# Kernel optimization log

Measured on AMD Instinct MI355X. Metric: run time of the kernel, lower is better.

## Reference

```python
import jax, jax.numpy as jnp
import numpy as np

N_NODES = 50000
N_EDGES = 600000
IN_CH = 300
HID = 128
N_CLASSES = 2
N_GRAPHS = 128
BN_EPS = 1e-5


def setup_inputs() -> dict:
    key = jax.random.key(0)
    ks = jax.random.split(key, 24)
    x = jax.random.normal(ks[0], (N_NODES, IN_CH), dtype=jnp.float32)
    edge_index = jax.random.randint(ks[1], (2, N_EDGES), 0, N_NODES, dtype=jnp.int64)
    batch = jnp.sort(jax.random.randint(ks[2], (N_NODES,), 0, N_GRAPHS, dtype=jnp.int64))

    def glorot(k, shape):
        fan_in, fan_out = shape
        s = jnp.sqrt(2.0 / (fan_in + fan_out)).astype(jnp.float32)
        return jax.random.normal(k, shape, dtype=jnp.float32) * s

    inp = {"x": x, "edge_index": edge_index, "batch": batch}
    # SAGEConv params: W_l (neighbor branch), W_r (root branch), bias
    dims = [(IN_CH, HID), (HID, HID), (HID, HID)]
    for i, (din, dout) in enumerate(dims, start=1):
        inp[f"W{i}l"] = glorot(ks[3 * i], (din, dout))
        inp[f"W{i}r"] = glorot(ks[3 * i + 1], (din, dout))
        inp[f"b{i}"] = jnp.zeros((dout,), dtype=jnp.float32)
        inp[f"g{i}"] = jnp.ones((dout,), dtype=jnp.float32)   # BN gamma
        inp[f"be{i}"] = jnp.zeros((dout,), dtype=jnp.float32)  # BN beta
    inp["Wc"] = glorot(ks[20], (HID, N_CLASSES))
    inp["bc"] = jnp.zeros((N_CLASSES,), dtype=jnp.float32)
    return inp


def _sage_conv(x, src, dst, Wl, Wr, b):
    # mean-aggregate neighbor features (messages flow src -> dst)
    msg_sum = jax.ops.segment_sum(x[src], dst, num_segments=N_NODES)
    deg = jax.ops.segment_sum(jnp.ones((src.shape[0],), dtype=x.dtype), dst,
                              num_segments=N_NODES)
    mean = msg_sum / jnp.maximum(deg, 1.0)[:, None]
    return mean @ Wl + x @ Wr + b


def _bn_relu(h, gamma, beta):
    mu = jnp.mean(h, axis=0)
    var = jnp.var(h, axis=0)
    h = (h - mu) * jax.lax.rsqrt(var + BN_EPS) * gamma + beta
    return jax.nn.relu(h)


def reference(x, edge_index, batch,
              W1l, W1r, b1, g1, be1,
              W2l, W2r, b2, g2, be2,
              W3l, W3r, b3, g3, be3,
              Wc, bc):
    src, dst = edge_index[0], edge_index[1]
    h = _bn_relu(_sage_conv(x, src, dst, W1l, W1r, b1), g1, be1)
    h = _bn_relu(_sage_conv(h, src, dst, W2l, W2r, b2), g2, be2)
    h = _bn_relu(_sage_conv(h, src, dst, W3l, W3r, b3), g3, be3)
    # global mean pool per graph
    pooled = jax.ops.segment_sum(h, batch, num_segments=N_GRAPHS)
    cnt = jax.ops.segment_sum(jnp.ones((h.shape[0],), dtype=h.dtype), batch,
                              num_segments=N_GRAPHS)
    hg = pooled / jnp.maximum(cnt, 1.0)[:, None]
    out = hg @ Wc + bc
    return out, hg
```

## Files before the change

kernel.cpp:

```cpp
#include <hip/hip_runtime.h>

#define N_NODES   50000
#define N_EDGES   600000
#define IN_CH     300
#define HID       128
#define N_CLASSES 2
#define N_GRAPHS  128
#define BN_EPS    1e-5f

#define NB ((N_NODES + 511) / 512)
#define KP1 320
#define NREP 32
#define DEGB ((N_EDGES + 255) / 256)
#define GEMMX_BLOCKS ((N_NODES + 63) / 64)
#define FILLB ((N_EDGES + 255) / 256)

typedef __attribute__((ext_vector_type(8))) short bf8_t;
typedef __attribute__((ext_vector_type(4))) float f4_t;

__device__ __forceinline__ unsigned short f2bf(float x) {
    union { float f; unsigned u; } q; q.f = x;
    unsigned r = q.u + 0x7fffu + ((q.u >> 16) & 1u);
    return (unsigned short)(r >> 16);
}
__device__ __forceinline__ float bf2f(unsigned short h) {
    union { float f; unsigned u; } q; q.u = ((unsigned)h) << 16; return q.f;
}

__global__ __launch_bounds__(256) void deg_prepw(const int* __restrict__ dst,
                                                 int* __restrict__ ideg,
                                                 const float* __restrict__ W1l,
                                                 const float* __restrict__ W1r,
                                                 const float* __restrict__ W2l,
                                                 const float* __restrict__ W2r,
                                                 const float* __restrict__ W3l,
                                                 const float* __restrict__ W3r,
                                                 unsigned short* __restrict__ B1h,
                                                 unsigned short* __restrict__ B1l,
                                                 unsigned short* __restrict__ B2h,
                                                 unsigned short* __restrict__ B2l,
                                                 unsigned short* __restrict__ B3h,
                                                 unsigned short* __restrict__ B3l) {
    int b = blockIdx.x;
    if (b < DEGB) {
        int e = b * 256 + threadIdx.x;
        if (e < N_EDGES) atomicAdd(&ideg[dst[e]], 1);
        return;
    }
    int pb = b - DEGB;
    int layer, base;
    if (pb < 320)      { layer = 0; base = pb; }
    else if (pb < 448) { layer = 1; base = pb - 320; }
    else               { layer = 2; base = pb - 448; }
    int Kp = (layer == 0) ? KP1 : HID;
    int K  = (layer == 0) ? IN_CH : HID;
    const float* Wl = (layer == 0) ? W1l : ((layer == 1) ? W2l : W3l);
    const float* Wr = (layer == 0) ? W1r : ((layer == 1) ? W2r : W3r);
    unsigned short* Bh = (layer == 0) ? B1h : ((layer == 1) ? B2h : B3h);
    unsigned short* Bl = (layer == 0) ? B1l : ((layer == 1) ? B2l : B3l);
    int idx = base * 256 + threadIdx.x;
    int n = idx / Kp;
    int k = idx - n * Kp;
    float v = 0.f;
    if (k < K) v = (n < 128) ? Wl[k * 128 + n] : Wr[k * 128 + (n - 128)];
    unsigned short h = f2bf(v);
    unsigned short l = f2bf(v - bf2f(h));
    int NST   = Kp >> 5;
    int ntile = n >> 4;
    int l16n  = n & 15;
    int kstep = k >> 5;
    int kk    = k & 31;
    int lane2 = (kk >> 3) * 16 + l16n;
    int addr  = ((ntile * NST + kstep) * 64 + lane2) * 8 + (kk & 7);
    Bh[addr] = h;
    Bl[addr] = l;
}

__global__ __launch_bounds__(256) void scan_fused(const int* __restrict__ ideg,
                                                  int* __restrict__ row_start,
                                                  float* __restrict__ invdeg,
                                                  int* __restrict__ bsum,
                                                  int* __restrict__ bflag) {
    int b = blockIdx.x, t = threadIdx.x;
    int lane = t & 63, wv = t >> 6;
    int i0 = b * 512 + t * 2;
    int v0 = 0, v1 = 0;
    if (i0 < N_NODES) {
        int2 v = *(const int2*)&ideg[i0];
        v0 = v.x; v1 = v.y;
    }
    int tot = v0 + v1;
    int s = tot;
#pragma unroll
    for (int d = 1; d < 64; d <<= 1) {
        int u = __shfl_up(s, d);
        if (lane >= d) s += u;
    }
    __shared__ int ws[4];
    if (lane == 63) ws[wv] = s;
    __syncthreads();
    int btot = ws[0] + ws[1] + ws[2] + ws[3];
    if (t == 0) {
        atomicExch(&bsum[b], btot);
        __threadfence();
        atomicExch(&bflag[b], 1);
    }
    int part = 0;
    if (t < b) {
        while (atomicAdd(&bflag[t], 0) == 0) {}
        part = atomicAdd(&bsum[t], 0);
    }
#pragma unroll
    for (int d = 1; d < 64; d <<= 1) part += __shfl_down(part, d);
    __shared__ int ps[4];
    if (lane == 0) ps[wv] = part;
    __syncthreads();
    int boff = ps[0] + ps[1] + ps[2] + ps[3];
    int woff = 0;
    for (int w = 0; w < wv; ++w) woff += ws[w];
    int base = boff + woff + (s - tot);
    if (i0 < N_NODES) {
        row_start[i0]     = base;
        row_start[i0 + 1] = base + v0;
        invdeg[i0]     = 1.0f / fmaxf((float)v0, 1.0f);
        invdeg[i0 + 1] = 1.0f / fmaxf((float)v1, 1.0f);
    }
    if (t == 0 && b == NB - 1) row_start[N_NODES] = boff + btot;
}

__global__ __launch_bounds__(256) void gemm_x_fill(const float* __restrict__ X,
                                                   int M,
                                                   const unsigned short* __restrict__ Bhi,
                                                   const unsigned short* __restrict__ Blo,
                                                   const float* __restrict__ bias,
                                                   unsigned short* __restrict__ C0,
                                                   float* __restrict__ C1,
                                                   const int* __restrict__ esrc,
                                                   const int* __restrict__ edst,
                                                   const int* __restrict__ row_start,
                                                   int* __restrict__ cursor,
                                                   int* __restrict__ csr_src) {
    if (blockIdx.x >= GEMMX_BLOCKS) {
        int e = (blockIdx.x - GEMMX_BLOCKS) * 256 + threadIdx.x;
        if (e < N_EDGES) {
            int d = edst[e];
            int pos = row_start[d] + atomicAdd(&cursor[d], 1);
            csr_src[pos] = esrc[e];
        }
        return;
    }

    __shared__ __align__(16) unsigned short sAh[2][64 * 32];
    __shared__ __align__(16) unsigned short sAl[2][64 * 32];

    const int tid  = threadIdx.x;
    const int lane = tid & 63;
    const int wave = tid >> 6;
    const int l16  = lane & 15;
    const int quad = lane >> 4;
    const long m0  = (long)blockIdx.x * 64;
    const int  n0  = wave * 64;

    f4_t acc[4][4];
#pragma unroll
    for (int mt = 0; mt < 4; ++mt)
#pragma unroll
        for (int nt = 0; nt < 4; ++nt) acc[mt][nt] = (f4_t){0.f, 0.f, 0.f, 0.f};

    const int ar  = tid >> 2;
    const int cl  = tid & 3;
    const int cpa = cl ^ ((ar >> 1) & 3);
    long agr = m0 + ar;
    if (agr >= M) agr = M - 1;
    const float* gX = X + agr * IN_CH;

    const int rsw = (quad ^ ((l16 >> 1) & 3)) * 8;
    const int NT  = KP1 / 32;

    const bf8_t* Bh0 = (const bf8_t*)Bhi;
    const bf8_t* Bl0 = (const bf8_t*)Blo;

    auto loadA = [&](int k0, float4& a0, float4& a1) {
        int gk = k0 + cl * 8;
        a0 = (gk + 4 <= IN_CH) ? *(const float4*)(gX + gk)
                               : make_float4(0.f, 0.f, 0.f, 0.f);
        a1 = (gk + 8 <= IN_CH) ? *(const float4*)(gX + gk + 4)
                               : make_float4(0.f, 0.f, 0.f, 0.f);
    };
    auto storeA = [&](int buf, float4 a0, float4 a1) {
        float f[8];
        f[0] = a0.x; f[1] = a0.y; f[2] = a0.z; f[3] = a0.w;
        f[4] = a1.x; f[5] = a1.y; f[6] = a1.z; f[7] = a1.w;
        bf8_t h8, l8;
#pragma unroll
        for (int j = 0; j < 8; ++j) {
            unsigned short h = f2bf(f[j]);
            h8[j] = (short)h;
            l8[j] = (short)f2bf(f[j] - bf2f(h));
        }
        *(bf8_t*)&sAh[buf][ar * 32 + cpa * 8] = h8;
        *(bf8_t*)&sAl[buf][ar * 32 + cpa * 8] = l8;
    };
    auto loadB = [&](int t, bf8_t (&bh)[4], bf8_t (&bl)[4]) {
#pragma unroll
        for (int nt = 0; nt < 4; ++nt) {
            long bi = ((long)(wave * 4 + nt) * NT + t) * 64 + lane;
            bh[nt] = Bh0[bi];
            bl[nt] = Bl0[bi];
        }
    };

    bf8_t bhv[4], blv[4];
    {
        float4 a0, a1;
        loadA(0, a0, a1);
        loadB(0, bhv, blv);
        storeA(0, a0, a1);
    }
    __syncthreads();

    int cur = 0;
    for (int t = 0; t < NT; ++t) {
        float4 na0 = make_float4(0.f, 0.f, 0.f, 0.f);
        float4 na1 = make_float4(0.f, 0.f, 0.f, 0.f);
        bf8_t nbh[4], nbl[4];
        const bool more = (t + 1 < NT);
        if (more) {
            loadA((t + 1) * 32, na0, na1);
            loadB(t + 1, nbh, nbl);
        }

        bf8_t ah[4], al[4];
#pragma unroll
        for (int mt = 0; mt < 4; ++mt) {
            ah[mt] = *(const bf8_t*)&sAh[cur][(mt * 16 + l16) * 32 + rsw];
            al[mt] = *(const bf8_t*)&sAl[cur][(mt * 16 + l16) * 32 + rsw];
        }
#pragma unroll
        for (int nt = 0; nt < 4; ++nt)
#pragma unroll
            for (int mt = 0; mt < 4; ++mt)
                acc[mt][nt] = __builtin_amdgcn_mfma_f32_16x16x32_bf16(ah[mt], bhv[nt], acc[mt][nt], 0, 0, 0);
#pragma unroll
        for (int nt = 0; nt < 4; ++nt)
#pragma unroll
            for (int mt = 0; mt < 4; ++mt)
                acc[mt][nt] = __builtin_amdgcn_mfma_f32_16x16x32_bf16(al[mt], bhv[nt], acc[mt][nt], 0, 0, 0);
#pragma unroll
        for (int nt = 0; nt < 4; ++nt)
#pragma unroll
            for (int mt = 0; mt < 4; ++mt)
                acc[mt][nt] = __builtin_amdgcn_mfma_f32_16x16x32_bf16(ah[mt], blv[nt], acc[mt][nt], 0, 0, 0);

        if (more) {
            storeA(cur ^ 1, na0, na1);
#pragma unroll
            for (int nt = 0; nt < 4; ++nt) {
                bhv[nt] = nbh[nt];
                blv[nt] = nbl[nt];
            }
        }
        __syncthreads();
        cur ^= 1;
    }

    const bool left = (n0 < 128);
    if (left) {
        int ncol[4];
#pragma unroll
        for (int nt = 0; nt < 4; ++nt) ncol[nt] = n0 + nt * 16 + l16;
#pragma unroll
        for (int mt = 0; mt < 4; ++mt)
#pragma unroll
            for (int r = 0; r < 4; ++r) {
                long row = m0 + mt * 16 + quad * 4 + r;
                if (row < M) {
#pragma unroll
                    for (int nt = 0; nt < 4; ++nt)
                        C0[row * 128 + ncol[nt]] = f2bf(acc[mt][nt][r]);
                }
            }
    } else {
        float badd[4];
        int   ncol[4];
#pragma unroll
        for (int nt = 0; nt < 4; ++nt) {
            int ng = n0 + nt * 16 + l16 - 128;
            ncol[nt] = ng;
            badd[nt] = bias[ng];
        }
#pragma unroll
        for (int mt = 0; mt < 4; ++mt)
#pragma unroll
            for (int r = 0; r < 4; ++r) {
                long row = m0 + mt * 16 + quad * 4 + r;
                if (row < M) {
#pragma unroll
                    for (int nt = 0; nt < 4; ++nt)
                        C1[row * 128 + ncol[nt]] = acc[mt][nt][r] + badd[nt];
                }
            }
    }
}

__global__ __launch_bounds__(256) void gemm_mfma_h(const float* __restrict__ Hpre,
                                                   int M,
                                                   const float* __restrict__ rep,
                                                   const float* __restrict__ gamma,
                                                   const float* __restrict__ beta,
                                                   const unsigned short* __restrict__ Bhi,
                                                   const unsigned short* __restrict__ Blo,
                                                   const float* __restrict__ bias,
                                                   unsigned short* __restrict__ C0,
                                                   float* __restrict__ C1) {
    __shared__ __align__(16) unsigned short sAh[2][64 * 32];
    __shared__ __align__(16) unsigned short sAl[2][64 * 32];
    __shared__ float sSC[256];

    const int tid  = threadIdx.x;
    const int lane = tid & 63;
    const int wave = tid >> 6;
    const int l16  = lane & 15;
    const int quad = lane >> 4;
    const long m0  = (long)blockIdx.x * 64;
    const int  n0  = wave * 64;

    {
        float* S = (float*)sAh;
        float a = 0.f;
#pragma unroll
        for (int r = 0; r < NREP; ++r) a += rep[r * 256 + tid];
        S[tid] = a;
        __syncthreads();
        if (tid < HID) {
            const float invn = 1.0f / (float)N_NODES;
            float mu  = S[tid] * invn;
            float var = S[HID + tid] * invn - mu * mu;
            float sc  = gamma[tid] * rsqrtf(var + BN_EPS);
            sSC[tid]       = sc;
            sSC[HID + tid] = beta[tid] - mu * sc;
        }
        __syncthreads();
    }

    f4_t acc[4][4];
#pragma unroll
    for (int mt = 0; mt < 4; ++mt)
#pragma unroll
        for (int nt = 0; nt < 4; ++nt) acc[mt][nt] = (f4_t){0.f, 0.f, 0.f, 0.f};

    const int ar  = tid >> 2;
    const int cl  = tid & 3;
    const int cpa = cl ^ ((ar >> 1) & 3);
    long agr = m0 + ar;
    if (agr >= M) agr = M - 1;
    const float* gH = Hpre + agr * HID;

    const int rsw = (quad ^ ((l16 >> 1) & 3)) * 8;
    const int NT  = HID / 32;

    const bf8_t* Bh0 = (const bf8_t*)Bhi;
    const bf8_t* Bl0 = (const bf8_t*)Blo;

    auto loadA = [&](int k0, float4& a0, float4& a1) {
        int gk = k0 + cl * 8;
        a0 = *(const float4*)(gH + gk);
        a1 = *(const float4*)(gH + gk + 4);
    };
    auto storeA = [&](int buf, int k0, float4 v0, float4 v1) {
        const int gk = k0 + cl * 8;
        float4 s0 = *(const float4*)&sSC[gk];
        float4 s1 = *(const float4*)&sSC[gk + 4];
        float4 t0 = *(const float4*)&sSC[HID + gk];
        float4 t1 = *(const float4*)&sSC[HID + gk + 4];
        float f[8];
        f[0] = fmaxf(v0.x * s0.x + t0.x, 0.f);
        f[1] = fmaxf(v0.y * s0.y + t0.y, 0.f);
        f[2] = fmaxf(v0.z * s0.z + t0.z, 0.f);
        f[3] = fmaxf(v0.w * s0.w + t0.w, 0.f);
        f[4] = fmaxf(v1.x * s1.x + t1.x, 0.f);
        f[5] = fmaxf(v1.y * s1.y + t1.y, 0.f);
        f[6] = fmaxf(v1.z * s1.z + t1.z, 0.f);
        f[7] = fmaxf(v1.w * s1.w + t1.w, 0.f);
        bf8_t h8, l8;
#pragma unroll
        for (int j = 0; j < 8; ++j) {
            unsigned short h = f2bf(f[j]);
            h8[j] = (short)h;
            l8[j] = (short)f2bf(f[j] - bf2f(h));
        }
        *(bf8_t*)&sAh[buf][ar * 32 + cpa * 8] = h8;
        *(bf8_t*)&sAl[buf][ar * 32 + cpa * 8] = l8;
    };
    auto loadB = [&](int t, bf8_t (&bh)[4], bf8_t (&bl)[4]) {
#pragma unroll
        for (int nt = 0; nt < 4; ++nt) {
            long bi = ((long)(wave * 4 + nt) * NT + t) * 64 + lane;
            bh[nt] = Bh0[bi];
            bl[nt] = Bl0[bi];
        }
    };

    bf8_t bhv[4], blv[4];
    {
        float4 a0, a1;
        loadA(0, a0, a1);
        loadB(0, bhv, blv);
        storeA(0, 0, a0, a1);
    }
    __syncthreads();

    int cur = 0;
#pragma unroll
    for (int t = 0; t < 4; ++t) {
        float4 na0 = make_float4(0.f, 0.f, 0.f, 0.f);
        float4 na1 = make_float4(0.f, 0.f, 0.f, 0.f);
        bf8_t nbh[4], nbl[4];
        const bool more = (t < 3);
        if (more) {
            loadA((t + 1) * 32, na0, na1);
            loadB(t + 1, nbh, nbl);
        }

        bf8_t ah[4], al[4];
#pragma unroll
        for (int mt = 0; mt < 4; ++mt) {
            ah[mt] = *(const bf8_t*)&sAh[cur][(mt * 16 + l16) * 32 + rsw];
            al[mt] = *(const bf8_t*)&sAl[cur][(mt * 16 + l16) * 32 + rsw];
        }
#pragma unroll
        for (int nt = 0; nt < 4; ++nt)
#pragma unroll
            for (int mt = 0; mt < 4; ++mt)
                acc[mt][nt] = __builtin_amdgcn_mfma_f32_16x16x32_bf16(ah[mt], bhv[nt], acc[mt][nt], 0, 0, 0);
#pragma unroll
        for (int nt = 0; nt < 4; ++nt)
#pragma unroll
            for (int mt = 0; mt < 4; ++mt)
                acc[mt][nt] = __builtin_amdgcn_mfma_f32_16x16x32_bf16(al[mt], bhv[nt], acc[mt][nt], 0, 0, 0);
#pragma unroll
        for (int nt = 0; nt < 4; ++nt)
#pragma unroll
            for (int mt = 0; mt < 4; ++mt)
                acc[mt][nt] = __builtin_amdgcn_mfma_f32_16x16x32_bf16(ah[mt], blv[nt], acc[mt][nt], 0, 0, 0);

        if (more) {
            storeA(cur ^ 1, (t + 1) * 32, na0, na1);
#pragma unroll
            for (int nt = 0; nt < 4; ++nt) {
                bhv[nt] = nbh[nt];
                blv[nt] = nbl[nt];
            }
        }
        __syncthreads();
        cur ^= 1;
    }

    const bool left = (n0 < 128);
    if (left) {
        int ncol[4];
#pragma unroll
        for (int nt = 0; nt < 4; ++nt) ncol[nt] = n0 + nt * 16 + l16;
#pragma unroll
        for (int mt = 0; mt < 4; ++mt)
#pragma unroll
            for (int r = 0; r < 4; ++r) {
                long row = m0 + mt * 16 + quad * 4 + r;
                if (row < M) {
#pragma unroll
                    for (int nt = 0; nt < 4; ++nt)
                        C0[row * 128 + ncol[nt]] = f2bf(acc[mt][nt][r]);
                }
            }
    } else {
        float badd[4];
        int   ncol[4];
#pragma unroll
        for (int nt = 0; nt < 4; ++nt) {
            int ng = n0 + nt * 16 + l16 - 128;
            ncol[nt] = ng;
            badd[nt] = bias[ng];
        }
#pragma unroll
        for (int mt = 0; mt < 4; ++mt)
#pragma unroll
            for (int r = 0; r < 4; ++r) {
                long row = m0 + mt * 16 + quad * 4 + r;
                if (row < M) {
#pragma unroll
                    for (int nt = 0; nt < 4; ++nt)
                        C1[row * 128 + ncol[nt]] = acc[mt][nt][r] + badd[nt];
                }
            }
    }
}

__global__ __launch_bounds__(256) void gather_agg(const unsigned short* __restrict__ Pl,
                                                  const int* __restrict__ row_start,
                                                  const int* __restrict__ csr_src,
                                                  const float* __restrict__ invdeg,
                                                  float* __restrict__ out,
                                                  float* __restrict__ rep) {
    int slot = threadIdx.x >> 5;
    int lane = threadIdx.x & 31;
    int node = blockIdx.x * 8 + slot;
    int beg = row_start[node];
    int end = row_start[node + 1];
    const unsigned short* base = Pl + lane * 4;
    float sx = 0.f, sy = 0.f, sz = 0.f, sw = 0.f;
    int j = beg;
    int deg = end - beg;

    if (deg > 0) {
        int n16 = (deg < 16) ? deg : 16;
        int idx[16];
#pragma unroll
        for (int u = 0; u < 16; ++u)
            idx[u] = csr_src[(u < n16) ? (j + u) : j];
        ushort4 v[16];
#pragma unroll
        for (int u = 0; u < 16; ++u)
            v[u] = *(const ushort4*)(base + (long)idx[u] * HID);
#pragma unroll
        for (int u = 0; u < 16; ++u) {
            float m = (u < n16) ? 1.f : 0.f;
            sx += m * bf2f(v[u].x); sy += m * bf2f(v[u].y);
            sz += m * bf2f(v[u].z); sw += m * bf2f(v[u].w);
        }
        j += n16;
    }
    for (; j + 8 <= end; j += 8) {
        int idx[8];
#pragma unroll
        for (int u = 0; u < 8; ++u) idx[u] = csr_src[j + u];
        ushort4 v[8];
#pragma unroll
        for (int u = 0; u < 8; ++u) v[u] = *(const ushort4*)(base + (long)idx[u] * HID);
#pragma unroll
        for (int u = 0; u < 8; ++u) {
            sx += bf2f(v[u].x); sy += bf2f(v[u].y);
            sz += bf2f(v[u].z); sw += bf2f(v[u].w);
        }
    }
    if (j + 4 <= end) {
        int idx[4];
#pragma unroll
        for (int u = 0; u < 4; ++u) idx[u] = csr_src[j + u];
        ushort4 v[4];
#pragma unroll
        for (int u = 0; u < 4; ++u) v[u] = *(const ushort4*)(base + (long)idx[u] * HID);
#pragma unroll
        for (int u = 0; u < 4; ++u) {
            sx += bf2f(v[u].x); sy += bf2f(v[u].y);
            sz += bf2f(v[u].z); sw += bf2f(v[u].w);
        }
        j += 4;
    }
    for (; j < end; ++j) {
        int i0 = csr_src[j];
        ushort4 v0 = *(const ushort4*)(base + (long)i0 * HID);
        sx += bf2f(v0.x); sy += bf2f(v0.y); sz += bf2f(v0.z); sw += bf2f(v0.w);
    }
    float w = invdeg[node];
    float* o = out + (long)node * HID + lane * 4;
    float4 cur = *(float4*)o;
    cur.x += sx * w;
    cur.y += sy * w;
    cur.z += sz * w;
    cur.w += sw * w;
    *(float4*)o = cur;

    __shared__ float red[8][HID];
    float* repb = rep + (blockIdx.x & (NREP - 1)) * 256;
    *(float4*)&red[slot][lane * 4] = make_float4(cur.x, cur.y, cur.z, cur.w);
    __syncthreads();
    if (threadIdx.x < HID) {
        float tsum = 0.f, tsq = 0.f;
#pragma unroll
        for (int s = 0; s < 8; ++s) {
            float v = red[s][threadIdx.x];
            tsum += v;
            tsq  += v * v;
        }
        atomicAdd(&repb[threadIdx.x], tsum);
        atomicAdd(&repb[HID + threadIdx.x], tsq);
    }
}

__global__ __launch_bounds__(1024) void poolhead_bn(const float* __restrict__ h,
                                                    const int* __restrict__ batch,
                                                    const float* __restrict__ rep,
                                                    const float* __restrict__ gamma,
                                                    const float* __restrict__ beta,
                                                    const float* __restrict__ Wc,
                                                    const float* __restrict__ bc,
                                                    float* __restrict__ out) {
    __shared__ float S[256];
    __shared__ float SC[256];
    int g = blockIdx.x;
    int t = threadIdx.x;
    int c = t & 127;
    int half = t >> 7;
    if (t < 256) {
        float a = 0.f;
#pragma unroll
        for (int r = 0; r < NREP; ++r) a += rep[r * 256 + t];
        S[t] = a;
    }
    __shared__ int lo_sh, hi_sh;
    if (t == 0) {
        int lo = 0, hi = N_NODES;
        while (lo < hi) { int m = (lo + hi) >> 1; if (batch[m] < g) lo = m + 1; else hi = m; }
        lo_sh = lo;
        int lo2 = lo, hi2 = N_NODES;
        while (lo2 < hi2) { int m = (lo2 + hi2) >> 1; if (batch[m] < g + 1) lo2 = m + 1; else hi2 = m; }
        hi_sh = lo2;
    }
    __syncthreads();
    if (t < HID) {
        const float invn = 1.0f / (float)N_NODES;
        float mu  = S[t] * invn;
        float var = S[HID + t] * invn - mu * mu;
        float sc  = gamma[t] * rsqrtf(var + BN_EPS);
        SC[t]       = sc;
        SC[HID + t] = beta[t] - mu * sc;
    }
    __syncthreads();
    float bsc = SC[c], bsh = SC[HID + c];
    int lo = lo_sh, hi = hi_sh;
    float a0 = 0.f, a1 = 0.f, a2 = 0.f, a3 = 0.f;
    int r = lo + half;
    for (; r + 24 < hi; r += 32) {
        a0 += fmaxf(h[(long)(r +  0) * HID + c] * bsc + bsh, 0.f);
        a1 += fmaxf(h[(long)(r +  8) * HID + c] * bsc + bsh, 0.f);
        a2 += fmaxf(h[(long)(r + 16) * HID + c] * bsc + bsh, 0.f);
        a3 += fmaxf(h[(long)(r + 24) * HID + c] * bsc + bsh, 0.f);
    }
    for (; r < hi; r += 8) a0 += fmaxf(h[(long)r * HID + c] * bsc + bsh, 0.f);
    __shared__ float red[8][HID];
    red[half][c] = (a0 + a1) + (a2 + a3);
    __syncthreads();
    __shared__ float r0[HID], r1[HID];
    if (t < HID) {
        float inv = 1.0f / fmaxf((float)(hi - lo), 1.0f);
        float v = 0.f;
#pragma unroll
        for (int s = 0; s < 8; ++s) v += red[s][t];
        v *= inv;
        out[N_GRAPHS * N_CLASSES + g * HID + t] = v;
        r0[t] = v * Wc[t * 2 + 0];
        r1[t] = v * Wc[t * 2 + 1];
    }
    __syncthreads();
    if (t < 2) {
        const float* rr = t ? r1 : r0;
        float sum = bc[t];
        for (int i = 0; i < HID; ++i) sum += rr[i];
        out[g * 2 + t] = sum;
    }
}

extern "C" void kernel_launch(void* const* d_in, const int* in_sizes, int n_in,
                              void* d_out, int out_size, void* d_ws, size_t ws_size,
                              hipStream_t stream) {
    const float* x     = (const float*)d_in[0];
    const int*   ei    = (const int*)d_in[1];
    const int*   batch = (const int*)d_in[2];
    const float* W1l = (const float*)d_in[3];
    const float* W1r = (const float*)d_in[4];
    const float* b1  = (const float*)d_in[5];
    const float* g1  = (const float*)d_in[6];
    const float* be1 = (const float*)d_in[7];
    const float* W2l = (const float*)d_in[8];
    const float* W2r = (const float*)d_in[9];
    const float* b2  = (const float*)d_in[10];
    const float* g2  = (const float*)d_in[11];
    const float* be2 = (const float*)d_in[12];
    const float* W3l = (const float*)d_in[13];
    const float* W3r = (const float*)d_in[14];
    const float* b3  = (const float*)d_in[15];
    const float* g3  = (const float*)d_in[16];
    const float* be3 = (const float*)d_in[17];
    const float* Wc  = (const float*)d_in[18];
    const float* bc  = (const float*)d_in[19];

    const int* src = ei;
    const int* dst = ei + N_EDGES;

    float* ws = (float*)d_ws;
    const long FEAT = (long)N_NODES * HID;
    unsigned short* Pl16 = (unsigned short*)ws;
    float* buf1 = ws + FEAT;
    float* buf2 = ws + 2 * FEAT;
    int*   ideg      = (int*)(ws + 3 * FEAT);
    int*   cursor    = ideg + N_NODES;
    int*   bsum      = cursor + N_NODES;
    int*   bflag     = bsum + 128;
    int*   row_start = bflag + 128;
    int*   csr_src   = row_start + N_NODES + 4;
    float* invdeg    = (float*)(csr_src + N_EDGES);
    float* reps      = invdeg + N_NODES;
    unsigned short* B1h = (unsigned short*)(reps + 3 * NREP * 256);
    unsigned short* B1l = B1h + 256 * KP1;
    unsigned short* B2h = B1l + 256 * KP1;
    unsigned short* B2l = B2h + 256 * HID;
    unsigned short* B3h = B2l + 256 * HID;
    unsigned short* B3l = B3h + 256 * HID;

    float* outp = (float*)d_out;

    const int gemm_grid   = (N_NODES + 63) / 64;
    const int gxf_grid    = GEMMX_BLOCKS + FILLB;
    const int gather_grid = N_NODES / 8;
    const int dp_grid     = DEGB + 320 + 128 + 128;

    hipMemsetAsync(ideg, 0, (2 * N_NODES + 256) * sizeof(int), stream);
    hipMemsetAsync(reps, 0, 3 * NREP * 256 * sizeof(float), stream);

    deg_prepw<<<dp_grid, 256, 0, stream>>>(dst, ideg, W1l, W1r, W2l, W2r, W3l, W3r,
                                           B1h, B1l, B2h, B2l, B3h, B3l);
    scan_fused<<<NB, 256, 0, stream>>>(ideg, row_start, invdeg, bsum, bflag);

    gemm_x_fill<<<gxf_grid, 256, 0, stream>>>(x, N_NODES, B1h, B1l, b1, Pl16, buf1,
                                              src, dst, row_start, cursor, csr_src);
    gather_agg<<<gather_grid, 256, 0, stream>>>(Pl16, row_start, csr_src, invdeg, buf1, reps);

    gemm_mfma_h<<<gemm_grid, 256, 0, stream>>>(buf1, N_NODES, reps, g1, be1,
                                               B2h, B2l, b2, Pl16, buf2);
    gather_agg<<<gather_grid, 256, 0, stream>>>(Pl16, row_start, csr_src, invdeg, buf2, reps + NREP * 256);

    gemm_mfma_h<<<gemm_grid, 256, 0, stream>>>(buf2, N_NODES, reps + NREP * 256, g2, be2,
                                               B3h, B3l, b3, Pl16, buf1);
    gather_agg<<<gather_grid, 256, 0, stream>>>(Pl16, row_start, csr_src, invdeg, buf1, reps + 2 * NREP * 256);

    poolhead_bn<<<N_GRAPHS, 1024, 0, stream>>>(buf1, batch, reps + 2 * NREP * 256,
                                               g3, be3, Wc, bc, outp);
}
```

Baseline: 356.6 us.

## Finalize BN stats in last gather block and widen gather to 16-byte loads

The gather kernel now uses 16 lanes per node with 8-wide bf16 loads, 16 nodes per block, so each lane moves more data per load. A completion counter lets the last gather block reduce the replicated BN statistics once and write scale/shift to global memory. The GEMM and pool kernels then read the precomputed scale/shift instead of each block re-reducing 32 replicas. This adds an atomic counter, a threadfence per block and a serial tail in one block, and the 4-wide tail loop is dropped.

```diff
diff --git a/kernel.cpp b/kernel.cpp
--- a/kernel.cpp
+++ b/kernel.cpp
@@ -14,6 +14,7 @@
 #define DEGB ((N_EDGES + 255) / 256)
 #define GEMMX_BLOCKS ((N_NODES + 63) / 64)
 #define FILLB ((N_EDGES + 255) / 256)
+#define GATB (N_NODES / 16)
 
 typedef __attribute__((ext_vector_type(8))) short bf8_t;
 typedef __attribute__((ext_vector_type(4))) float f4_t;
@@ -305,9 +306,7 @@
 
 __global__ __launch_bounds__(256) void gemm_mfma_h(const float* __restrict__ Hpre,
                                                    int M,
-                                                   const float* __restrict__ rep,
-                                                   const float* __restrict__ gamma,
-                                                   const float* __restrict__ beta,
+                                                   const float* __restrict__ SCg,
                                                    const unsigned short* __restrict__ Bhi,
                                                    const unsigned short* __restrict__ Blo,
                                                    const float* __restrict__ bias,
@@ -325,23 +324,7 @@
     const long m0  = (long)blockIdx.x * 64;
     const int  n0  = wave * 64;
 
-    {
-        float* S = (float*)sAh;
-        float a = 0.f;
-#pragma unroll
-        for (int r = 0; r < NREP; ++r) a += rep[r * 256 + tid];
-        S[tid] = a;
-        __syncthreads();
-        if (tid < HID) {
-            const float invn = 1.0f / (float)N_NODES;
-            float mu  = S[tid] * invn;
-            float var = S[HID + tid] * invn - mu * mu;
-            float sc  = gamma[tid] * rsqrtf(var + BN_EPS);
-            sSC[tid]       = sc;
-            sSC[HID + tid] = beta[tid] - mu * sc;
-        }
-        __syncthreads();
-    }
+    sSC[tid] = SCg[tid];
 
     f4_t acc[4][4];
 #pragma unroll
@@ -406,6 +389,7 @@
         float4 a0, a1;
         loadA(0, a0, a1);
         loadB(0, bhv, blv);
+        __syncthreads();
         storeA(0, 0, a0, a1);
     }
     __syncthreads();
@@ -500,14 +484,20 @@
                                                   const int* __restrict__ csr_src,
                                                   const float* __restrict__ invdeg,
                                                   float* __restrict__ out,
-                                                  float* __restrict__ rep) {
-    int slot = threadIdx.x >> 5;
-    int lane = threadIdx.x & 31;
-    int node = blockIdx.x * 8 + slot;
+                                                  float* __restrict__ rep,
+                                                  const float* __restrict__ gamma,
+                                                  const float* __restrict__ beta,
+                                                  float* __restrict__ SCg,
+                                                  int* __restrict__ dcnt) {
+    int slot = threadIdx.x >> 4;
+    int lane = threadIdx.x & 15;
+    int node = blockIdx.x * 16 + slot;
     int beg = row_start[node];
     int end = row_start[node + 1];
-    const unsigned short* base = Pl + lane * 4;
-    float sx = 0.f, sy = 0.f, sz = 0.f, sw = 0.f;
+    const unsigned short* base = Pl + lane * 8;
+    float s[8];
+#pragma unroll
+    for (int i = 0; i < 8; ++i) s[i] = 0.f;
     int j = beg;
     int deg = end - beg;
 
@@ -517,15 +507,16 @@
 #pragma unroll
         for (int u = 0; u < 16; ++u)
             idx[u] = csr_src[(u < n16) ? (j + u) : j];
-        ushort4 v[16];
+        bf8_t v[16];
 #pragma unroll
         for (int u = 0; u < 16; ++u)
-            v[u] = *(const ushort4*)(base + (long)idx[u] * HID);
+            v[u] = *(const bf8_t*)(base + (long)idx[u] * HID);
 #pragma unroll
         for (int u = 0; u < 16; ++u) {
             float m = (u < n16) ? 1.f : 0.f;
-            sx += m * bf2f(v[u].x); sy += m * bf2f(v[u].y);
-            sz += m * bf2f(v[u].z); sw += m * bf2f(v[u].w);
+#pragma unroll
+            for (int i = 0; i < 8; ++i)
+                s[i] += m * bf2f((unsigned short)v[u][i]);
         }
         j += n16;
     }
@@ -533,80 +524,87 @@
         int idx[8];
 #pragma unroll
         for (int u = 0; u < 8; ++u) idx[u] = csr_src[j + u];
-        ushort4 v[8];
-#pragma unroll
-        for (int u = 0; u < 8; ++u) v[u] = *(const ushort4*)(base + (long)idx[u] * HID);
-#pragma unroll
-        for (int u = 0; u < 8; ++u) {
-            sx += bf2f(v[u].x); sy += bf2f(v[u].y);
-            sz += bf2f(v[u].z); sw += bf2f(v[u].w);
-        }
-    }
-    if (j + 4 <= end) {
-        int idx[4];
-#pragma unroll
-        for (int u = 0; u < 4; ++u) idx[u] = csr_src[j + u];
-        ushort4 v[4];
-#pragma unroll
-        for (int u = 0; u < 4; ++u) v[u] = *(const ushort4*)(base + (long)idx[u] * HID);
-#pragma unroll
-        for (int u = 0; u < 4; ++u) {
-            sx += bf2f(v[u].x); sy += bf2f(v[u].y);
-            sz += bf2f(v[u].z); sw += bf2f(v[u].w);
-        }
-        j += 4;
+        bf8_t v[8];
+#pragma unroll
+        for (int u = 0; u < 8; ++u) v[u] = *(const bf8_t*)(base + (long)idx[u] * HID);
+#pragma unroll
+        for (int u = 0; u < 8; ++u)
+#pragma unroll
+            for (int i = 0; i < 8; ++i)
+                s[i] += bf2f((unsigned short)v[u][i]);
     }
     for (; j < end; ++j) {
         int i0 = csr_src[j];
-        ushort4 v0 = *(const ushort4*)(base + (long)i0 * HID);
-        sx += bf2f(v0.x); sy += bf2f(v0.y); sz += bf2f(v0.z); sw += bf2f(v0.w);
+        bf8_t v0 = *(const bf8_t*)(base + (long)i0 * HID);
+#pragma unroll
+        for (int i = 0; i < 8; ++i) s[i] += bf2f((unsigned short)v0[i]);
     }
     float w = invdeg[node];
-    float* o = out + (long)node * HID + lane * 4;
-    float4 cur = *(float4*)o;
-    cur.x += sx * w;
-    cur.y += sy * w;
-    cur.z += sz * w;
-    cur.w += sw * w;
-    *(float4*)o = cur;
-
-    __shared__ float red[8][HID];
+    float* o = out + (long)node * HID + lane * 8;
+    float4 c0 = *(float4*)o;
+    float4 c1 = *(float4*)(o + 4);
+    c0.x += s[0] * w; c0.y += s[1] * w; c0.z += s[2] * w; c0.w += s[3] * w;
+    c1.x += s[4] * w; c1.y += s[5] * w; c1.z += s[6] * w; c1.w += s[7] * w;
+    *(float4*)o       = c0;
+    *(float4*)(o + 4) = c1;
+
+    __shared__ float red[16][HID];
     float* repb = rep + (blockIdx.x & (NREP - 1)) * 256;
-    *(float4*)&red[slot][lane * 4] = make_float4(cur.x, cur.y, cur.z, cur.w);
+    *(float4*)&red[slot][lane * 8]     = c0;
+    *(float4*)&red[slot][lane * 8 + 4] = c1;
     __syncthreads();
     if (threadIdx.x < HID) {
         float tsum = 0.f, tsq = 0.f;
 #pragma unroll
-        for (int s = 0; s < 8; ++s) {
-            float v = red[s][threadIdx.x];
+        for (int ss = 0; ss < 16; ++ss) {
+            float v = red[ss][threadIdx.x];
             tsum += v;
             tsq  += v * v;
         }
         atomicAdd(&repb[threadIdx.x], tsum);
         atomicAdd(&repb[HID + threadIdx.x], tsq);
     }
+
+    __syncthreads();
+    __shared__ int isLast;
+    if (threadIdx.x == 0) {
+        __threadfence();
+        int d = atomicAdd(dcnt, 1);
+        isLast = (d == GATB - 1);
+    }
+    __syncthreads();
+    if (isLast) {
+        int t = threadIdx.x;
+        volatile const float* vrep = rep;
+        float a = 0.f;
+#pragma unroll
+        for (int r = 0; r < NREP; ++r) a += vrep[r * 256 + t];
+        __shared__ float S[256];
+        S[t] = a;
+        __syncthreads();
+        if (t < HID) {
+            const float invn = 1.0f / (float)N_NODES;
+            float mu  = S[t] * invn;
+            float var = S[HID + t] * invn - mu * mu;
+            float sc  = gamma[t] * rsqrtf(var + BN_EPS);
+            SCg[t]       = sc;
+            SCg[HID + t] = beta[t] - mu * sc;
+        }
+    }
 }
 
 __global__ __launch_bounds__(1024) void poolhead_bn(const float* __restrict__ h,
                                                     const int* __restrict__ batch,
-                                                    const float* __restrict__ rep,
-                                                    const float* __restrict__ gamma,
-                                                    const float* __restrict__ beta,
+                                                    const float* __restrict__ SCg,
                                                     const float* __restrict__ Wc,
                                                     const float* __restrict__ bc,
                                                     float* __restrict__ out) {
-    __shared__ float S[256];
     __shared__ float SC[256];
     int g = blockIdx.x;
     int t = threadIdx.x;
     int c = t & 127;
     int half = t >> 7;
-    if (t < 256) {
-        float a = 0.f;
-#pragma unroll
-        for (int r = 0; r < NREP; ++r) a += rep[r * 256 + t];
-        S[t] = a;
-    }
+    if (t < 256) SC[t] = SCg[t];
     __shared__ int lo_sh, hi_sh;
     if (t == 0) {
         int lo = 0, hi = N_NODES;
@@ -615,15 +613,6 @@
         int lo2 = lo, hi2 = N_NODES;
         while (lo2 < hi2) { int m = (lo2 + hi2) >> 1; if (batch[m] < g + 1) lo2 = m + 1; else hi2 = m; }
         hi_sh = lo2;
-    }
-    __syncthreads();
-    if (t < HID) {
-        const float invn = 1.0f / (float)N_NODES;
-        float mu  = S[t] * invn;
-        float var = S[HID + t] * invn - mu * mu;
-        float sc  = gamma[t] * rsqrtf(var + BN_EPS);
-        SC[t]       = sc;
-        SC[HID + t] = beta[t] - mu * sc;
     }
     __syncthreads();
     float bsc = SC[c], bsh = SC[HID + c];
@@ -700,7 +689,11 @@
     int*   csr_src   = row_start + N_NODES + 4;
     float* invdeg    = (float*)(csr_src + N_EDGES);
     float* reps      = invdeg + N_NODES;
-    unsigned short* B1h = (unsigned short*)(reps + 3 * NREP * 256);
+    float* SC1g      = reps + 3 * NREP * 256;
+    float* SC2g      = SC1g + 256;
+    float* SC3g      = SC2g + 256;
+    int*   dcnt      = (int*)(SC3g + 256);
+    unsigned short* B1h = (unsigned short*)(dcnt + 4);
     unsigned short* B1l = B1h + 256 * KP1;
     unsigned short* B2h = B1l + 256 * KP1;
     unsigned short* B2l = B2h + 256 * HID;
@@ -711,11 +704,10 @@
 
     const int gemm_grid   = (N_NODES + 63) / 64;
     const int gxf_grid    = GEMMX_BLOCKS + FILLB;
-    const int gather_grid = N_NODES / 8;
     const int dp_grid     = DEGB + 320 + 128 + 128;
 
     hipMemsetAsync(ideg, 0, (2 * N_NODES + 256) * sizeof(int), stream);
-    hipMemsetAsync(reps, 0, 3 * NREP * 256 * sizeof(float), stream);
+    hipMemsetAsync(reps, 0, (3 * NREP * 256 + 3 * 256 + 4) * sizeof(float), stream);
 
     deg_prepw<<<dp_grid, 256, 0, stream>>>(dst, ideg, W1l, W1r, W2l, W2r, W3l, W3r,
                                            B1h, B1l, B2h, B2l, B3h, B3l);
@@ -723,16 +715,18 @@
 
     gemm_x_fill<<<gxf_grid, 256, 0, stream>>>(x, N_NODES, B1h, B1l, b1, Pl16, buf1,
                                               src, dst, row_start, cursor, csr_src);
-    gather_agg<<<gather_grid, 256, 0, stream>>>(Pl16, row_start, csr_src, invdeg, buf1, reps);
-
-    gemm_mfma_h<<<gemm_grid, 256, 0, stream>>>(buf1, N_NODES, reps, g1, be1,
+    gather_agg<<<GATB, 256, 0, stream>>>(Pl16, row_start, csr_src, invdeg, buf1, reps,
+                                         g1, be1, SC1g, dcnt + 0);
+
+    gemm_mfma_h<<<gemm_grid, 256, 0, stream>>>(buf1, N_NODES, SC1g,
                                                B2h, B2l, b2, Pl16, buf2);
-    gather_agg<<<gather_grid, 256, 0, stream>>>(Pl16, row_start, csr_src, invdeg, buf2, reps + NREP * 256);
-
-    gemm_mfma_h<<<gemm_grid, 256, 0, stream>>>(buf2, N_NODES, reps + NREP * 256, g2, be2,
+    gather_agg<<<GATB, 256, 0, stream>>>(Pl16, row_start, csr_src, invdeg, buf2,
+                                         reps + NREP * 256, g2, be2, SC2g, dcnt + 1);
+
+    gemm_mfma_h<<<gemm_grid, 256, 0, stream>>>(buf2, N_NODES, SC2g,
                                                B3h, B3l, b3, Pl16, buf1);
-    gather_agg<<<gather_grid, 256, 0, stream>>>(Pl16, row_start, csr_src, invdeg, buf1, reps + 2 * NREP * 256);
-
-    poolhead_bn<<<N_GRAPHS, 1024, 0, stream>>>(buf1, batch, reps + 2 * NREP * 256,
-                                               g3, be3, Wc, bc, outp);
-}
+    gather_agg<<<GATB, 256, 0, stream>>>(Pl16, row_start, csr_src, invdeg, buf1,
+                                         reps + 2 * NREP * 256, g3, be3, SC3g, dcnt + 2);
+
+    poolhead_bn<<<N_GRAPHS, 1024, 0, stream>>>(buf1, batch, SC3g, Wc, bc, outp);
+}
```

Result: slower. 711.6 us (+99.5%).
